# Kernel optimization log

Measured on AMD Instinct MI355X. Metric: run time of the kernel, lower is better.

The kernel has to match this reference:

```python
import jax, jax.numpy as jnp
import numpy as np

NUM_SAMPLES = 1024


def _cdist(a, b):
    # a, b: (n, 3) -> (n, n) pairwise euclidean distances (torch.cdist p=2)
    d2 = jnp.sum((a[:, None, :] - b[None, :, :]) ** 2, axis=-1)
    return jnp.sqrt(jnp.maximum(d2, 0.0))


def _greedy_match_cost(cost):
    # Greedy sequential matching: repeatedly take the global argmin over
    # still-unmatched rows/cols, accumulate its cost, eliminate row+col.
    n = cost.shape[0]

    def step(carry, _):
        row_mask, col_mask, loss = carry
        valid = row_mask[:, None] & col_mask[None, :]
        masked = jnp.where(valid, cost, jnp.inf)
        idx = jnp.argmin(masked)  # row-major first-min == torch's min(dim=1)+argmin tiebreak
        r = idx // n
        c = idx % n
        loss = loss + cost[r, c]
        return (row_mask.at[r].set(False), col_mask.at[c].set(False), loss), None

    init = (jnp.ones((n,), dtype=bool), jnp.ones((n,), dtype=bool), jnp.float32(0.0))
    (_, _, loss), _ = jax.lax.scan(step, init, None, length=n)
    return loss / n


def setup_inputs() -> dict:
    key = jax.random.key(0)
    k1, k2, k3 = jax.random.split(key, 3)
    B, N, n = 8, 4096, NUM_SAMPLES
    S1 = jax.random.normal(k1, (B, N, 3), dtype=jnp.float32)
    S2 = jax.random.normal(k2, (B, N, 3), dtype=jnp.float32)
    # torch.randperm(N)[:n] per batch element: without-replacement sampling
    perm_keys = jax.random.split(k3, B)
    indices = jax.vmap(lambda k: jax.random.permutation(k, N)[:n])(perm_keys).astype(jnp.int32)
    return {"S1": S1, "S2": S2, "indices": indices}


def reference(S1, S2, indices):
    # sample the same indices from both sets, per batch (matches original loop)
    s1 = jnp.take_along_axis(S1, indices[:, :, None], axis=1)  # (B, n, 3)
    s2 = jnp.take_along_axis(S2, indices[:, :, None], axis=1)  # (B, n, 3)
    cost = jax.vmap(_cdist)(s1, s2)  # (B, n, n)
    losses = jax.vmap(_greedy_match_cost)(cost)  # (B,)
    return jnp.mean(losses)
```

## Files before the change

kernel.cpp:

```cpp
#include <hip/hip_runtime.h>
#include <stdint.h>

#define BATCH 8
#define NPTS 4096
#define NS 1024
#define KD 6

typedef unsigned long long u64;
typedef unsigned int u32;
typedef unsigned short u16;
typedef unsigned char u8;

#define DEADV (~0ull)
#define QNANB 0x7FC00000u

__device__ __forceinline__ float pdist3(float ax, float ay, float az,
                                        float bx, float by, float bz) {
    float dx = ax - bx, dy = ay - by, dz = az - bz;
    float d2 = __fmaf_rn(dz, dz, __fmaf_rn(dy, dy, dx * dx));
    return __fsqrt_rn(d2);
}

__device__ __forceinline__ u64 packv(float d, u32 row, u32 col) {
    return ((u64)__float_as_uint(d) << 20) | ((u64)row << 10) | (u64)col;
}

__device__ __forceinline__ u64 u64min2(u64 a, u64 b) { return a < b ? a : b; }
__device__ __forceinline__ u64 u64max2(u64 a, u64 b) { return a > b ? a : b; }

__device__ __forceinline__ u64 tree16(const u64* p) {
    u64 a0 = u64min2(p[0], p[1]),   a1 = u64min2(p[2], p[3]);
    u64 a2 = u64min2(p[4], p[5]),   a3 = u64min2(p[6], p[7]);
    u64 a4 = u64min2(p[8], p[9]),   a5 = u64min2(p[10], p[11]);
    u64 a6 = u64min2(p[12], p[13]), a7 = u64min2(p[14], p[15]);
    u64 b0 = u64min2(a0, a1), b1 = u64min2(a2, a3);
    u64 b2 = u64min2(a4, a5), b3 = u64min2(a6, a7);
    return u64min2(u64min2(b0, b1), u64min2(b2, b3));
}

template<int CTRL>
__device__ __forceinline__ u64 dpp_min_step(u64 m) {
    u32 lo = (u32)m, hi = (u32)(m >> 32);
    u32 olo = (u32)__builtin_amdgcn_update_dpp(-1, (int)lo, CTRL, 0xF, 0xF, false);
    u32 ohi = (u32)__builtin_amdgcn_update_dpp(-1, (int)hi, CTRL, 0xF, 0xF, false);
    u64 o = ((u64)ohi << 32) | olo;
    return o < m ? o : m;
}

__device__ __forceinline__ u64 wave_min_u64(u64 m) {
    m = dpp_min_step<0x111>(m);
    m = dpp_min_step<0x112>(m);
    m = dpp_min_step<0x114>(m);
    m = dpp_min_step<0x118>(m);
    m = dpp_min_step<0x142>(m);
    m = dpp_min_step<0x143>(m);
    u32 lo = (u32)__builtin_amdgcn_readlane((int)(u32)m, 63);
    u32 hi = (u32)__builtin_amdgcn_readlane((int)(u32)(m >> 32), 63);
    return ((u64)hi << 32) | lo;
}

__global__ void gather_k(const float* __restrict__ S1, const float* __restrict__ S2,
                         const int* __restrict__ idx,
                         float4* __restrict__ s1g, float4* __restrict__ s2g,
                         int* __restrict__ cnt) {
    int t = blockIdx.x * blockDim.x + threadIdx.x;
    if (t == 0) *cnt = 0;
    if (t >= BATCH * NS) return;
    int b = t >> 10;
    int j = idx[t];
    const float* p1 = S1 + ((size_t)b * NPTS + j) * 3;
    const float* p2 = S2 + ((size_t)b * NPTS + j) * 3;
    s1g[t] = make_float4(p1[0], p1[1], p1[2], 0.f);
    s2g[t] = make_float4(p2[0], p2[1], p2[2], 0.f);
}

__global__ void lists_k(const float4* __restrict__ s1g, const float4* __restrict__ s2g,
                        u64* __restrict__ rlist_g, u64* __restrict__ clist_g) {
    __shared__ float4 pts[NS];
    int gg = blockIdx.x * 4 + (threadIdx.x >> 6);
    int lane = threadIdx.x & 63;
    int side = (gg >= BATCH * NS) ? 1 : 0;
    int g = gg - side * (BATCH * NS);
    int b = g >> 10;
    u32 rc = (u32)(g & 1023);
    const float4* other = (side ? s1g : s2g) + (size_t)b * NS;
    for (int i = threadIdx.x; i < NS; i += 256) pts[i] = other[i];
    float4 a = side ? s2g[g] : s1g[g];
    __syncthreads();
    u64 cand[16];
    #pragma unroll
    for (int k = 0; k < 16; ++k) {
        int o = lane + (k << 6);
        float4 q = pts[o];
        float d = pdist3(a.x, a.y, a.z, q.x, q.y, q.z);
        cand[k] = side ? packv(d, (u32)o, rc) : packv(d, rc, (u32)o);
    }
    u64* out = (side ? clist_g : rlist_g) + (size_t)g * KD;
    for (int i = 0; i < KD; ++i) {
        u64 m1 = wave_min_u64(tree16(cand));
        if (lane == 0) out[i] = m1;
        #pragma unroll
        for (int k = 0; k < 16; ++k) cand[k] = (cand[k] == m1) ? DEADV : cand[k];
    }
}

__global__ void __launch_bounds__(1024, 1)
resolve_k(const float4* __restrict__ s1g, const float4* __restrict__ s2g,
          const u64* __restrict__ rlist_gl, const u64* __restrict__ clist_gl,
          float* __restrict__ loss_ws, int* __restrict__ cnt,
          float* __restrict__ out, u64* __restrict__ instr) {
    __shared__ u64 rlist[NS * KD];
    __shared__ u64 clist[NS * KD];
    __shared__ u64 rmin[NS];
    __shared__ u64 cmin[NS];
    __shared__ float4 s1p[NS];
    __shared__ float4 s2p[NS];
    __shared__ u8 rptrs[NS], cptrs[NS];
    __shared__ u16 qrow[NS], qcol[NS];
    __shared__ u16 lrows[NS], lcols[NS];
    __shared__ float lred[1024];
    __shared__ int qrn, qcn, matched, nlr, nlc, stale_n;
    int b = blockIdx.x;
    int tid = threadIdx.x;
    int lane = tid & 63, wv = tid >> 6;

    {
        const float4* rs = (const float4*)(rlist_gl + (size_t)b * NS * KD);
        const float4* cs = (const float4*)(clist_gl + (size_t)b * NS * KD);
        float4* rd = (float4*)rlist;
        float4* cd = (float4*)clist;
        for (int i = tid; i < NS * KD / 2; i += 1024) { rd[i] = rs[i]; cd[i] = cs[i]; }
    }
    s1p[tid] = s1g[(size_t)b * NS + tid];
    s2p[tid] = s2g[(size_t)b * NS + tid];
    rptrs[tid] = 1; cptrs[tid] = 1;
    lrows[tid] = (u16)tid; lcols[tid] = (u16)tid;
    if (tid == 0) { matched = 0; stale_n = NS; }
    __syncthreads();
    rmin[tid] = rlist[tid * KD];
    cmin[tid] = clist[tid * KD];
    float loss = 0.f;
    __syncthreads();

    long long tmark = 0;
    u64 sA = 0, sB = 0;
    if (tid == 0) tmark = clock64();

    for (int round = 0; round < NS; ++round) {
        u64 myk = rmin[tid];
        u32 c = (u32)myk & 1023u;
        bool mut = (myk != DEADV) && (cmin[c] == myk);
        if (mut) {
            loss += __uint_as_float((u32)(myk >> 20));
            rmin[tid] = DEADV;
            cmin[c] = DEADV;
            s1p[tid].x = __uint_as_float(QNANB);
            s2p[c].x   = __uint_as_float(QNANB);
        }
        u64 bal = __ballot((int)mut);
        if (lane == 0 && bal) atomicAdd(&matched, (int)__popcll(bal));
        if (tid == 0) { qrn = 0; qcn = 0; nlr = 0; nlc = 0; }
        __syncthreads();
        if (tid == 0) { long long t = clock64(); sA += (u64)(t - tmark); tmark = t; }
        int m = matched;
        if (m >= NS) break;
        int live = NS - m;
        int stale = stale_n;
        bool rebuild = (stale * 4 > live * 5 + 64);
        bool needR = false, needC = false;
        u64 rk = rmin[tid];
        if (rk != DEADV) {
            float pr = s2p[(u32)rk & 1023u].x;
            if (pr != pr) {
                u32 p = rptrs[tid];
                bool found = false;
                while (p < KD) {
                    u64 e = rlist[tid * KD + p];
                    ++p;
                    if (e != DEADV) {
                        float q = s2p[(u32)e & 1023u].x;
                        if (q == q) { rmin[tid] = e; found = true; break; }
                    }
                }
                rptrs[tid] = (u8)p;
                needR = !found;
            }
        }
        u64 ck = cmin[tid];
        if (ck != DEADV) {
            float pr = s1p[((u32)ck >> 10) & 1023u].x;
            if (pr != pr) {
                u32 p = cptrs[tid];
                bool found = false;
                while (p < KD) {
                    u64 e = clist[tid * KD + p];
                    ++p;
                    if (e != DEADV) {
                        float q = s1p[((u32)e >> 10) & 1023u].x;
                        if (q == q) { cmin[tid] = e; found = true; break; }
                    }
                }
                cptrs[tid] = (u8)p;
                needC = !found;
            }
        }
        {
            u64 rb2 = __ballot((int)needR);
            if (rb2) {
                int rrank = (int)__popcll(rb2 & ((1ull << lane) - 1ull));
                int rbase = 0;
                if (lane == 0) rbase = atomicAdd(&qrn, (int)__popcll(rb2));
                rbase = __shfl(rbase, 0, 64);
                if (needR) qrow[rbase + rrank] = (u16)tid;
            }
            u64 cb2 = __ballot((int)needC);
            if (cb2) {
                int crank = (int)__popcll(cb2 & ((1ull << lane) - 1ull));
                int cbase = 0;
                if (lane == 0) cbase = atomicAdd(&qcn, (int)__popcll(cb2));
                cbase = __shfl(cbase, 0, 64);
                if (needC) qcol[cbase + crank] = (u16)tid;
            }
        }
        if (rebuild) {
            float cx = s2p[tid].x;
            bool calive = (cx == cx);
            u64 cb = __ballot((int)calive);
            int crank = (int)__popcll(cb & ((1ull << lane) - 1ull));
            int cbase = 0;
            if (lane == 0) cbase = atomicAdd(&nlc, (int)__popcll(cb));
            cbase = __shfl(cbase, 0, 64);
            if (calive) lcols[cbase + crank] = (u16)tid;

            float rx = s1p[tid].x;
            bool ralive = (rx == rx);
            u64 rb = __ballot((int)ralive);
            int rrank = (int)__popcll(rb & ((1ull << lane) - 1ull));
            int rbase = 0;
            if (lane == 0) rbase = atomicAdd(&nlr, (int)__popcll(rb));
            rbase = __shfl(rbase, 0, 64);
            if (ralive) lrows[rbase + rrank] = (u16)tid;
        }
        __syncthreads();
        if (tid == 0) { long long t = clock64(); sB += (u64)(t - tmark); tmark = t; }
        int nr = qrn, nc = qcn;
        int scan_n = rebuild ? live : stale;
        if (rebuild && tid == 0) stale_n = live;
        int tot = nr + nc;
        for (int qi = wv; qi < tot; qi += 16) {
            if (qi < nr) {
                u32 r = qrow[qi];
                float4 a = s1p[r];
                u64 m1 = DEADV, m2 = DEADV;
                for (int i = lane; i < scan_n; i += 64) {
                    int cc = lcols[i];
                    float4 q = s2p[cc];
                    float d = pdist3(a.x, a.y, a.z, q.x, q.y, q.z);
                    u64 p = packv(d, r, (u32)cc);
                    u64 mx = u64max2(p, m1);
                    m1 = u64min2(m1, p);
                    m2 = u64min2(m2, mx);
                }
                u64 M1 = wave_min_u64(m1);
                u64 c2 = (m1 == M1) ? m2 : m1;
                u64 M2 = wave_min_u64(c2);
                if (lane == 0) {
                    rmin[r] = M1;
                    rlist[r * KD + KD - 1] = M2;
                    rptrs[r] = KD - 1;
                }
            } else {
                u32 cc = qcol[qi - nr];
                float4 a = s2p[cc];
                u64 m1 = DEADV, m2 = DEADV;
                for (int i = lane; i < scan_n; i += 64) {
                    int r = lrows[i];
                    float4 q = s1p[r];
                    float d = pdist3(q.x, q.y, q.z, a.x, a.y, a.z);
                    u64 p = packv(d, (u32)r, cc);
                    u64 mx = u64max2(p, m1);
                    m1 = u64min2(m1, p);
                    m2 = u64min2(m2, mx);
                }
                u64 M1 = wave_min_u64(m1);
                u64 c2 = (m1 == M1) ? m2 : m1;
                u64 M2 = wave_min_u64(c2);
                if (lane == 0) {
                    cmin[cc] = M1;
                    clist[cc * KD + KD - 1] = M2;
                    cptrs[cc] = KD - 1;
                }
            }
        }
        __syncthreads();
        if (tid == 0) tmark = clock64();
    }

    if (instr && b == 0 && tid == 0) {
        u64 n1 = sA >> 13; if (n1 > 63) n1 = 63;
        u64 n2 = sB >> 13; if (n2 > 63) n2 = 63;
        int n = (int)(n1 * 64 + n2);
        for (int k = 0; k < n; ++k)
            __builtin_nontemporal_store(0ull, instr + (size_t)k * 8);
    }

    lred[tid] = loss;
    __syncthreads();
    #pragma unroll
    for (int s = 512; s > 0; s >>= 1) {
        if (tid < s) lred[tid] += lred[tid + s];
        __syncthreads();
    }
    if (tid == 0) {
        atomicExch(&loss_ws[b], lred[0] * (1.0f / NS));
        __threadfence();
        int old = atomicAdd(cnt, 1);
        if (old == BATCH - 1) {
            __threadfence();
            float s = 0.f;
            for (int i = 0; i < BATCH; ++i) s += atomicAdd(&loss_ws[i], 0.0f);
            out[0] = s * (1.0f / BATCH);
        }
    }
}

extern "C" void kernel_launch(void* const* d_in, const int* in_sizes, int n_in,
                              void* d_out, int out_size, void* d_ws, size_t ws_size,
                              hipStream_t stream) {
    const float* S1 = (const float*)d_in[0];
    const float* S2 = (const float*)d_in[1];
    const int* idx  = (const int*)d_in[2];
    char* ws = (char*)d_ws;
    size_t o = 0;
    float4* s1g    = (float4*)(ws + o); o += (size_t)BATCH * NS * 16;
    float4* s2g    = (float4*)(ws + o); o += (size_t)BATCH * NS * 16;
    u64* rlist_g   = (u64*)(ws + o);    o += (size_t)BATCH * NS * KD * 8;
    u64* clist_g   = (u64*)(ws + o);    o += (size_t)BATCH * NS * KD * 8;
    float* loss_ws = (float*)(ws + o);  o += (size_t)BATCH * 4;
    int* cnt       = (int*)(ws + o);    o += 64;
    o = (o + 4095) & ~(size_t)4095;
    u64* instr     = (u64*)(ws + o);
    o += (size_t)4096 * 64;
    u64* instr_p = (ws_size >= o) ? instr : (u64*)0;

    gather_k<<<(BATCH * NS + 255) / 256, 256, 0, stream>>>(S1, S2, idx, s1g, s2g, cnt);
    lists_k<<<2 * BATCH * NS / 4, 256, 0, stream>>>(s1g, s2g, rlist_g, clist_g);
    resolve_k<<<BATCH, 1024, 0, stream>>>(s1g, s2g, rlist_g, clist_g, loss_ws, cnt,
                                          (float*)d_out, instr_p);
}
```

Measured before the change: 200.8 us.

## Transpose candidate lists, replace shared atomics with per-wave counters, unroll rescans

Candidate lists move from row-major [row][k] to k-major [k][row] layout, both in global memory and in LDS, so that each thread's lookups are strided by row and avoid bank conflicts. The shared atomic counters for matched and queue sizes are replaced by per-wave counts that every thread sums locally, and the rescan queue is split into per-wave segments that are located by a prefix walk. The rescan inner loop is unrolled four ways to expose more parallel LDS loads. This trades a little extra per-thread arithmetic for fewer atomics and fewer bank conflicts inside a latency-bound serial loop.

Measured after the change: 250.7 us. 1.25x slower.

```diff
diff --git a/kernel.cpp b/kernel.cpp
--- a/kernel.cpp
+++ b/kernel.cpp
@@ -95,10 +95,10 @@
         float d = pdist3(a.x, a.y, a.z, q.x, q.y, q.z);
         cand[k] = side ? packv(d, (u32)o, rc) : packv(d, rc, (u32)o);
     }
-    u64* out = (side ? clist_g : rlist_g) + (size_t)g * KD;
+    u64* out = (side ? clist_g : rlist_g) + (size_t)b * NS * KD + rc;
     for (int i = 0; i < KD; ++i) {
         u64 m1 = wave_min_u64(tree16(cand));
-        if (lane == 0) out[i] = m1;
+        if (lane == 0) out[(size_t)i * NS] = m1;
         #pragma unroll
         for (int k = 0; k < 16; ++k) cand[k] = (cand[k] == m1) ? DEADV : cand[k];
     }
@@ -109,17 +109,18 @@
           const u64* __restrict__ rlist_gl, const u64* __restrict__ clist_gl,
           float* __restrict__ loss_ws, int* __restrict__ cnt,
           float* __restrict__ out, u64* __restrict__ instr) {
-    __shared__ u64 rlist[NS * KD];
-    __shared__ u64 clist[NS * KD];
+    __shared__ u64 rlist[KD * NS];
+    __shared__ u64 clist[KD * NS];
     __shared__ u64 rmin[NS];
     __shared__ u64 cmin[NS];
     __shared__ float4 s1p[NS];
     __shared__ float4 s2p[NS];
     __shared__ u8 rptrs[NS], cptrs[NS];
-    __shared__ u16 qrow[NS], qcol[NS];
+    __shared__ u16 qrowW[16 * 64], qcolW[16 * 64];
+    __shared__ int qrnW[16], qcnW[16], mcnt[16];
     __shared__ u16 lrows[NS], lcols[NS];
     __shared__ float lred[1024];
-    __shared__ int qrn, qcn, matched, nlr, nlc, stale_n;
+    __shared__ int nlr, nlc, stale_n;
     int b = blockIdx.x;
     int tid = threadIdx.x;
     int lane = tid & 63, wv = tid >> 6;
@@ -135,11 +136,12 @@
     s2p[tid] = s2g[(size_t)b * NS + tid];
     rptrs[tid] = 1; cptrs[tid] = 1;
     lrows[tid] = (u16)tid; lcols[tid] = (u16)tid;
-    if (tid == 0) { matched = 0; stale_n = NS; }
+    if (tid == 0) stale_n = NS;
     __syncthreads();
-    rmin[tid] = rlist[tid * KD];
-    cmin[tid] = clist[tid * KD];
+    rmin[tid] = rlist[tid];
+    cmin[tid] = clist[tid];
     float loss = 0.f;
+    int m_reg = 0;
     __syncthreads();
 
     long long tmark = 0;
@@ -158,13 +160,18 @@
             s2p[c].x   = __uint_as_float(QNANB);
         }
         u64 bal = __ballot((int)mut);
-        if (lane == 0 && bal) atomicAdd(&matched, (int)__popcll(bal));
-        if (tid == 0) { qrn = 0; qcn = 0; nlr = 0; nlc = 0; }
+        if (lane == 0) mcnt[wv] = (int)__popcll(bal);
+        if (tid == 0) { nlr = 0; nlc = 0; }
         __syncthreads();
         if (tid == 0) { long long t = clock64(); sA += (u64)(t - tmark); tmark = t; }
-        int m = matched;
-        if (m >= NS) break;
-        int live = NS - m;
+        {
+            int rs = 0;
+            #pragma unroll
+            for (int j = 0; j < 16; ++j) rs += mcnt[j];
+            m_reg += rs;
+        }
+        if (m_reg >= NS) break;
+        int live = NS - m_reg;
         int stale = stale_n;
         bool rebuild = (stale * 4 > live * 5 + 64);
         bool needR = false, needC = false;
@@ -175,7 +182,7 @@
                 u32 p = rptrs[tid];
                 bool found = false;
                 while (p < KD) {
-                    u64 e = rlist[tid * KD + p];
+                    u64 e = rlist[p * NS + tid];
                     ++p;
                     if (e != DEADV) {
                         float q = s2p[(u32)e & 1023u].x;
@@ -193,7 +200,7 @@
                 u32 p = cptrs[tid];
                 bool found = false;
                 while (p < KD) {
-                    u64 e = clist[tid * KD + p];
+                    u64 e = clist[p * NS + tid];
                     ++p;
                     if (e != DEADV) {
                         float q = s1p[((u32)e >> 10) & 1023u].x;
@@ -206,21 +213,13 @@
         }
         {
             u64 rb2 = __ballot((int)needR);
-            if (rb2) {
-                int rrank = (int)__popcll(rb2 & ((1ull << lane) - 1ull));
-                int rbase = 0;
-                if (lane == 0) rbase = atomicAdd(&qrn, (int)__popcll(rb2));
-                rbase = __shfl(rbase, 0, 64);
-                if (needR) qrow[rbase + rrank] = (u16)tid;
-            }
+            int rrank = (int)__popcll(rb2 & ((1ull << lane) - 1ull));
+            if (needR) qrowW[(wv << 6) + rrank] = (u16)tid;
+            if (lane == 0) qrnW[wv] = (int)__popcll(rb2);
             u64 cb2 = __ballot((int)needC);
-            if (cb2) {
-                int crank = (int)__popcll(cb2 & ((1ull << lane) - 1ull));
-                int cbase = 0;
-                if (lane == 0) cbase = atomicAdd(&qcn, (int)__popcll(cb2));
-                cbase = __shfl(cbase, 0, 64);
-                if (needC) qcol[cbase + crank] = (u16)tid;
-            }
+            int crank = (int)__popcll(cb2 & ((1ull << lane) - 1ull));
+            if (needC) qcolW[(wv << 6) + crank] = (u16)tid;
+            if (lane == 0) qcnW[wv] = (int)__popcll(cb2);
         }
         if (rebuild) {
             float cx = s2p[tid].x;
@@ -243,51 +242,83 @@
         }
         __syncthreads();
         if (tid == 0) { long long t = clock64(); sB += (u64)(t - tmark); tmark = t; }
-        int nr = qrn, nc = qcn;
         int scan_n = rebuild ? live : stale;
         if (rebuild && tid == 0) stale_n = live;
-        int tot = nr + nc;
+        int cR[16], cC[16];
+        #pragma unroll
+        for (int j = 0; j < 16; ++j) { cR[j] = qrnW[j]; cC[j] = qcnW[j]; }
+        int totR = 0, totC = 0;
+        #pragma unroll
+        for (int j = 0; j < 16; ++j) { totR += cR[j]; totC += cC[j]; }
+        int tot = totR + totC;
         for (int qi = wv; qi < tot; qi += 16) {
-            if (qi < nr) {
-                u32 r = qrow[qi];
+            bool isRow = qi < totR;
+            int x = isRow ? qi : qi - totR;
+            int seg = 0, base = 0, acc = 0;
+            #pragma unroll
+            for (int j = 0; j < 16; ++j) {
+                acc += isRow ? cR[j] : cC[j];
+                bool adv = (x >= acc);
+                seg  = adv ? j + 1 : seg;
+                base = adv ? acc : base;
+            }
+            int local = x - base;
+            if (isRow) {
+                u32 r = qrowW[(seg << 6) + local];
                 float4 a = s1p[r];
                 u64 m1 = DEADV, m2 = DEADV;
-                for (int i = lane; i < scan_n; i += 64) {
-                    int cc = lcols[i];
-                    float4 q = s2p[cc];
-                    float d = pdist3(a.x, a.y, a.z, q.x, q.y, q.z);
-                    u64 p = packv(d, r, (u32)cc);
-                    u64 mx = u64max2(p, m1);
-                    m1 = u64min2(m1, p);
-                    m2 = u64min2(m2, mx);
+                for (int i = lane; i < scan_n; i += 256) {
+                    int i1 = i + 64, i2 = i + 128, i3 = i + 192;
+                    int x0 = lcols[i];
+                    int x1 = lcols[i1 < scan_n ? i1 : i];
+                    int x2 = lcols[i2 < scan_n ? i2 : i];
+                    int x3 = lcols[i3 < scan_n ? i3 : i];
+                    float4 q0 = s2p[x0], q1 = s2p[x1], q2 = s2p[x2], q3 = s2p[x3];
+                    u64 p0 = packv(pdist3(a.x, a.y, a.z, q0.x, q0.y, q0.z), r, (u32)x0);
+                    u64 p1 = (i1 < scan_n) ? packv(pdist3(a.x, a.y, a.z, q1.x, q1.y, q1.z), r, (u32)x1) : DEADV;
+                    u64 p2 = (i2 < scan_n) ? packv(pdist3(a.x, a.y, a.z, q2.x, q2.y, q2.z), r, (u32)x2) : DEADV;
+                    u64 p3 = (i3 < scan_n) ? packv(pdist3(a.x, a.y, a.z, q3.x, q3.y, q3.z), r, (u32)x3) : DEADV;
+                    u64 mx;
+                    mx = u64max2(p0, m1); m1 = u64min2(m1, p0); m2 = u64min2(m2, mx);
+                    mx = u64max2(p1, m1); m1 = u64min2(m1, p1); m2 = u64min2(m2, mx);
+                    mx = u64max2(p2, m1); m1 = u64min2(m1, p2); m2 = u64min2(m2, mx);
+                    mx = u64max2(p3, m1); m1 = u64min2(m1, p3); m2 = u64min2(m2, mx);
                 }
                 u64 M1 = wave_min_u64(m1);
                 u64 c2 = (m1 == M1) ? m2 : m1;
                 u64 M2 = wave_min_u64(c2);
                 if (lane == 0) {
                     rmin[r] = M1;
-                    rlist[r * KD + KD - 1] = M2;
+                    rlist[(KD - 1) * NS + r] = M2;
                     rptrs[r] = KD - 1;
                 }
             } else {
-                u32 cc = qcol[qi - nr];
+                u32 cc = qcolW[(seg << 6) + local];
                 float4 a = s2p[cc];
                 u64 m1 = DEADV, m2 = DEADV;
-                for (int i = lane; i < scan_n; i += 64) {
-                    int r = lrows[i];
-                    float4 q = s1p[r];
-                    float d = pdist3(q.x, q.y, q.z, a.x, a.y, a.z);
-                    u64 p = packv(d, (u32)r, cc);
-                    u64 mx = u64max2(p, m1);
-                    m1 = u64min2(m1, p);
-                    m2 = u64min2(m2, mx);
+                for (int i = lane; i < scan_n; i += 256) {
+                    int i1 = i + 64, i2 = i + 128, i3 = i + 192;
+                    int x0 = lrows[i];
+                    int x1 = lrows[i1 < scan_n ? i1 : i];
+                    int x2 = lrows[i2 < scan_n ? i2 : i];
+                    int x3 = lrows[i3 < scan_n ? i3 : i];
+                    float4 q0 = s1p[x0], q1 = s1p[x1], q2 = s1p[x2], q3 = s1p[x3];
+                    u64 p0 = packv(pdist3(q0.x, q0.y, q0.z, a.x, a.y, a.z), (u32)x0, cc);
+                    u64 p1 = (i1 < scan_n) ? packv(pdist3(q1.x, q1.y, q1.z, a.x, a.y, a.z), (u32)x1, cc) : DEADV;
+                    u64 p2 = (i2 < scan_n) ? packv(pdist3(q2.x, q2.y, q2.z, a.x, a.y, a.z), (u32)x2, cc) : DEADV;
+                    u64 p3 = (i3 < scan_n) ? packv(pdist3(q3.x, q3.y, q3.z, a.x, a.y, a.z), (u32)x3, cc) : DEADV;
+                    u64 mx;
+                    mx = u64max2(p0, m1); m1 = u64min2(m1, p0); m2 = u64min2(m2, mx);
+                    mx = u64max2(p1, m1); m1 = u64min2(m1, p1); m2 = u64min2(m2, mx);
+                    mx = u64max2(p2, m1); m1 = u64min2(m1, p2); m2 = u64min2(m2, mx);
+                    mx = u64max2(p3, m1); m1 = u64min2(m1, p3); m2 = u64min2(m2, mx);
                 }
                 u64 M1 = wave_min_u64(m1);
                 u64 c2 = (m1 == M1) ? m2 : m1;
                 u64 M2 = wave_min_u64(c2);
                 if (lane == 0) {
                     cmin[cc] = M1;
-                    clist[cc * KD + KD - 1] = M2;
+                    clist[(KD - 1) * NS + cc] = M2;
                     cptrs[cc] = KD - 1;
                 }
             }
```
